# Kernel optimization log

Hardware: AMD Instinct MI355X
Metric: run time of the kernel (lower is better)

The kernel has to match this reference:

```python
import jax, jax.numpy as jnp
import numpy as np

C = 512
H_HEADS = 8  # self-attn heads (num_heads) and cross-attn heads (n_heads), both 8


def _self_attn(x, Wq, Wkv):
    # x: [B,N,C]; shared (ModuleParallel) linear weights, qkv_bias=False
    B, N, _ = x.shape
    h, d = H_HEADS, C // H_HEADS
    q = (x @ Wq.T).reshape(B, N, h, d).transpose(0, 2, 1, 3)          # [B,h,N,d]
    kv = (x @ Wkv.T).reshape(B, N, 2, h, d).transpose(2, 0, 3, 1, 4)  # [2,B,h,N,d]
    k, v = kv[0], kv[1]
    attn = jax.nn.softmax(jnp.einsum('bhnd,bhmd->bhnm', q, k) * (d ** -0.5), axis=-1)
    y = jnp.einsum('bhnm,bhmd->bhnd', attn, v).transpose(0, 2, 1, 3).reshape(B, N, C)
    return y


def _judger(y_self, y_other, Wj1, bj1, Wj2, bj2):
    # Mlp_2(2C->C->C) with exact GELU, then softmax over channel dim
    hdn = jax.nn.gelu(jnp.concatenate([y_self, y_other], axis=-1) @ Wj1.T + bj1, approximate=False)
    return jax.nn.softmax(hdn @ Wj2.T + bj2, axis=-1)


def _cross_attn(yq, ykv, kn_row, vn_row, Win, bin_, Wout, bout, rel):
    # Vectorized form of the per-sample loop: each token is a seq-len-1 query
    # attending over 2 keys: [noise_k + yq, yq * relation_score].
    B, N, _ = yq.shape
    h, d = H_HEADS, C // H_HEADS
    qw, kw, vw = Win[:C], Win[C:2 * C], Win[2 * C:]
    bq, bk, bv = bin_[:C], bin_[C:2 * C], bin_[2 * C:]
    k_in = jnp.stack([kn_row + yq, yq * rel], axis=-2)   # [B,N,2,C]
    v_in = jnp.stack([vn_row + yq, ykv], axis=-2)        # [B,N,2,C]
    qp = (yq @ qw.T + bq).reshape(B, N, h, d)
    kp = (k_in @ kw.T + bk).reshape(B, N, 2, h, d)
    vp = (v_in @ vw.T + bv).reshape(B, N, 2, h, d)
    scores = jnp.einsum('bnhd,bnkhd->bnhk', qp, kp) * (d ** -0.5)
    w = jax.nn.softmax(scores, axis=-1)
    o = jnp.einsum('bnhk,bnkhd->bnhd', w, vp).reshape(B, N, C)
    return o @ Wout.T + bout


def setup_inputs() -> dict:
    key = jax.random.key(0)
    ks = jax.random.split(key, 16)
    B, N = 8, 1024
    s = 0.02
    inp = {
        'x0': jax.random.normal(ks[0], (B, N, C), jnp.float32),
        'x1': jax.random.normal(ks[1], (B, N, C), jnp.float32),
        'H': 32, 'W': 32,
        'Wq': jax.random.normal(ks[2], (C, C), jnp.float32) * s,
        'Wkv': jax.random.normal(ks[3], (2 * C, C), jnp.float32) * s,
        'Wj1': jax.random.normal(ks[4], (C, 2 * C), jnp.float32) * s,
        'bj1': jnp.zeros((C,), jnp.float32),
        'Wj2': jax.random.normal(ks[5], (C, C), jnp.float32) * s,
        'bj2': jnp.zeros((C,), jnp.float32),
        'kn': jax.random.normal(ks[6], (2, C), jnp.float32),
        'vn': jax.random.normal(ks[7], (2, C), jnp.float32),
        'Wc0_in': jax.random.normal(ks[8], (3 * C, C), jnp.float32) * s,
        'bc0_in': jnp.zeros((3 * C,), jnp.float32),
        'Wc0_out': jax.random.normal(ks[9], (C, C), jnp.float32) * s,
        'bc0_out': jnp.zeros((C,), jnp.float32),
        'Wc1_in': jax.random.normal(ks[10], (3 * C, C), jnp.float32) * s,
        'bc1_in': jnp.zeros((3 * C,), jnp.float32),
        'Wc1_out': jax.random.normal(ks[11], (C, C), jnp.float32) * s,
        'bc1_out': jnp.zeros((C,), jnp.float32),
        'Wp': jax.random.normal(ks[12], (C, C), jnp.float32) * s,
        'bp': jnp.zeros((C,), jnp.float32),
    }
    return inp


def reference(x0, x1, H, W, Wq, Wkv, Wj1, bj1, Wj2, bj2, kn, vn,
              Wc0_in, bc0_in, Wc0_out, bc0_out, Wc1_in, bc1_in, Wc1_out, bc1_out,
              Wp, bp):
    # Dual self-attention (shared q/kv projections across modalities, sr_ratio=1)
    y0 = _self_attn(x0, Wq, Wkv)
    y1 = _self_attn(x1, Wq, Wkv)
    # Noise-augmented relation-gated cross-attention (vectorized over batch)
    rel0 = _judger(y0, y1, Wj1, bj1, Wj2, bj2)
    rel1 = _judger(y1, y0, Wj1, bj1, Wj2, bj2)
    new0 = y0 + _cross_attn(y0, y1, kn[0], vn[0], Wc0_in, bc0_in, Wc0_out, bc0_out, rel0)
    new1 = y1 + _cross_attn(y1, y0, kn[1], vn[1], Wc1_in, bc1_in, Wc1_out, bc1_out, rel1)
    out0 = new0 @ Wp.T + bp
    out1 = new1 @ Wp.T + bp
    return jnp.stack([out0, out1])  # [2,B,N,C]
```

## Files before the change

### kernel.cpp

```cpp
#include <hip/hip_runtime.h>

typedef unsigned short u16;
typedef u16 u16x8 __attribute__((ext_vector_type(8)));
typedef __bf16 bf16x8 __attribute__((ext_vector_type(8)));
typedef __bf16 bf16x2 __attribute__((ext_vector_type(2)));
typedef float f32x4 __attribute__((ext_vector_type(4)));

__device__ __forceinline__ float b2f(u16 h) {
  union { unsigned u; float f; } x; x.u = ((unsigned)h) << 16; return x.f;
}
__device__ __forceinline__ u16 f2b(float f) {
  union { float f; unsigned u; } x; x.f = f;
  unsigned r = x.u + 0x7FFFu + ((x.u >> 16) & 1u);
  return (u16)(r >> 16);
}
__device__ __forceinline__ f32x4 mfma16(bf16x8 a, bf16x8 b, f32x4 c) {
  return __builtin_amdgcn_mfma_f32_16x16x32_bf16(a, b, c, 0, 0, 0);
}
__device__ __forceinline__ void gload16(const void* g, void* l) {
  __builtin_amdgcn_global_load_lds(
      (const __attribute__((address_space(1))) void*)g,
      (__attribute__((address_space(3))) void*)l, 16, 0, 0);
}
#define WAITV8 asm volatile("s_waitcnt vmcnt(8)" ::: "memory")
#define WAITV4 asm volatile("s_waitcnt vmcnt(4)" ::: "memory")
#define WAITV0 asm volatile("s_waitcnt vmcnt(0)" ::: "memory")
#define WAITL0 asm volatile("s_waitcnt lgkmcnt(0)" ::: "memory")
#define BARRIER asm volatile("s_barrier" ::: "memory")

__global__ __launch_bounds__(256) void xcvt_k(const float* __restrict__ x0,
                                              const float* __restrict__ x1,
                                              u16* __restrict__ out) {
  int b = blockIdx.x;
  const float* src = (b < 4096) ? x0 : x1;
  u16* dst = out + (b < 4096 ? 0 : 4194304);
  int i = (b & 4095) * 1024 + threadIdx.x * 4;
  float4 v = *(const float4*)&src[i];
  dst[i + 0] = f2b(v.x); dst[i + 1] = f2b(v.y);
  dst[i + 2] = f2b(v.z); dst[i + 3] = f2b(v.w);
}

__global__ __launch_bounds__(256) void wcvt_k(
    const float* __restrict__ wq, const float* __restrict__ wkv,
    const float* __restrict__ wj1, const float* __restrict__ wj2,
    const float* __restrict__ wci0, const float* __restrict__ wci1,
    const float* __restrict__ wp, u16* __restrict__ wsb) {
  int b = blockIdx.x; const float* src; size_t doff; int lb;
  if      (b < 256)  { src = wq;   doff = 0;       lb = b; }
  else if (b < 768)  { src = wkv;  doff = 262144;  lb = b - 256; }
  else if (b < 1280) { src = wj1;  doff = 786432;  lb = b - 768; }
  else if (b < 1536) { src = wj2;  doff = 1310720; lb = b - 1280; }
  else if (b < 2304) { src = wci0; doff = 1572864; lb = b - 1536; }
  else if (b < 3072) { src = wci1; doff = 2359296; lb = b - 2304; }
  else               { src = wp;   doff = 3145728; lb = b - 3072; }
  int i = lb * 1024 + threadIdx.x * 4;
  float4 v = *(const float4*)&src[i];
  u16* dst = wsb + doff + i;
  u16 c0 = f2b(v.x), c1 = f2b(v.y), c2 = f2b(v.z), c3 = f2b(v.w);
  dst[0] = c0; dst[1] = c1; dst[2] = c2; dst[3] = c3;
  if (b >= 3072) {
    int row = i >> 9, col = i & 511;
    u16* f0 = wsb + 3932160 + (size_t)row * 1024 + col;
    u16* f1 = wsb + 4456448 + (size_t)row * 1024 + col;
    f0[0] = c0; f0[1] = c1; f0[2] = c2; f0[3] = c3;
    f1[0] = c0; f1[1] = c1; f1[2] = c2; f1[3] = c3;
  }
}

__global__ __launch_bounds__(256) void tcvt_k(const float* __restrict__ w0,
                                              const float* __restrict__ w1,
                                              u16* __restrict__ o0,
                                              u16* __restrict__ o1) {
  __shared__ u16 t[64][65];
  const int b = blockIdx.x;
  const float* src = (b & 64) ? w1 : w0;
  u16* dst = (b & 64) ? o1 : o0;
  const int r0 = ((b >> 3) & 7) * 64, c0 = (b & 7) * 64;
  const int tid = threadIdx.x;
#pragma unroll
  for (int i = 0; i < 16; i++) {
    int idx = tid + i * 256;
    int r = idx >> 6, c = idx & 63;
    t[r][c] = f2b(src[(size_t)(r0 + r) * 512 + c0 + c]);
  }
  __syncthreads();
#pragma unroll
  for (int i = 0; i < 16; i++) {
    int idx = tid + i * 256;
    int c = idx >> 6, r = idx & 63;
    dst[(size_t)(c0 + c) * 512 + r0 + r] = t[r][c];
  }
}

__global__ __launch_bounds__(256) void cvec_k(
    const float* __restrict__ kn, const float* __restrict__ vn,
    const float* __restrict__ bp, const float* __restrict__ bco0,
    const float* __restrict__ bco1, const u16* __restrict__ wci0,
    const u16* __restrict__ wci1, const u16* __restrict__ wp,
    float* __restrict__ out) {
  int idx = blockIdx.x * 256 + threadIdx.x;
  int which = idx >> 9, col = idx & 511;
  const float* src; const u16* w; float acc;
  if (which < 4) {
    int s = which & 1, isv = which >> 1;
    src = (isv ? vn : kn) + s * 512;
    w = (s ? wci1 : wci0) + (isv ? 524288 : 262144) + (size_t)col * 512;
    acc = 0.f;
  } else {
    int s = which & 1;
    src = s ? bco1 : bco0;
    w = wp + (size_t)col * 512;
    acc = bp[col];
  }
  for (int k = 0; k < 512; k += 8) {
    u16x8 w8 = *(const u16x8*)&w[k];
#pragma unroll
    for (int j = 0; j < 8; j++) acc += src[k + j] * b2f(w8[j]);
  }
  out[idx] = acc;
}

template<int EPI, int AMODE>
__global__ __launch_bounds__(256, 3) void gemm6_k(
    const u16* __restrict__ A, int astr, int K1, int K,
    const u16* __restrict__ W0, const u16* __restrict__ W1,
    const float* __restrict__ b0, const float* __restrict__ b1,
    void* __restrict__ outp, int ostr, int ncol) {
  __shared__ u16 SM[32768];
  const int tid = threadIdx.x, lane = tid & 63, wv = tid >> 6;
  const int wr = wv >> 1, wc = wv & 1;
  const int lr = lane & 15, lg = lane >> 4;
  const int L = blockIdx.x;
  const int nrow = gridDim.x / ncol;
  int row_b, col_b;
  if ((nrow & 7) == 0) {
    int xcd = L & 7, s = L >> 3;
    row_b = xcd * (nrow >> 3) + s / ncol;
    col_b = s % ncol;
  } else { row_b = L % nrow; col_b = L / nrow; }
  const int row0 = row_b * 128, col0 = col_b * 128;
  const int strm = (row0 >= 8192) ? 1 : 0;
  const u16* W = strm ? W1 : W0;
  const float* bias = strm ? b1 : b0;
  const int shift = (AMODE == 4 && col0 >= 1536) ? 512 : 0;
  const int cxor  = (AMODE == 4 && col0 >= 1536) ? 8192 : 0;
  const int bcl = (lane & 7) * 16;

  f32x4 acc[4][4];
#pragma unroll
  for (int m = 0; m < 4; m++)
#pragma unroll
    for (int n = 0; n < 4; n++) acc[m][n] = f32x4{0.f, 0.f, 0.f, 0.f};

  const int nk = K >> 6;

  auto stage = [&](int k0, int buf) {
    const int Ab = buf * 16384, Wb = buf * 16384 + 8192;
#pragma unroll
    for (int ch = 0; ch < 4; ch++) {
      int r = ch * 32 + (tid >> 3);
      int bcs = bcl ^ ((r & 7) << 4);
      const char* asrc;
      if constexpr (AMODE == 3) {
        if (k0 < K1)
          asrc = (const char*)(A + (size_t)(row0 + r) * astr) + k0 * 2 + bcs;
        else
          asrc = (const char*)(A + (size_t)((row0 + r) ^ 8192) * astr) +
                 (k0 - K1) * 2 + bcs;
      } else {
        asrc = (const char*)(A + (size_t)((row0 + r) ^ cxor) * astr) +
               k0 * 2 + bcs;
      }
      gload16(asrc, &SM[Ab + (ch * 32 + wv * 8) * 64]);
      const char* wsrc =
          (const char*)(W + (size_t)(col0 - shift + r) * K) + k0 * 2 + bcs;
      gload16(wsrc, &SM[Wb + (ch * 32 + wv * 8) * 64]);
    }
  };

  stage(0, 0);
  for (int t = 0; t < nk; t++) {
    const int buf = t & 1;
    if (t + 1 < nk) {
      stage((t + 1) * 64, buf ^ 1);
      WAITV8;
    } else {
      WAITV0;
    }
    BARRIER;
    const int Ab = buf * 16384, Wb = buf * 16384 + 8192;
#pragma unroll
    for (int kk = 0; kk < 2; kk++) {
      const int c = kk * 32 + lg * 8;
      bf16x8 af[4], wf[4];
#pragma unroll
      for (int m = 0; m < 4; m++) {
        int r = wr * 64 + m * 16 + lr;
        af[m] = *(const bf16x8*)&SM[Ab + r * 64 + (c ^ ((r & 7) << 3))];
      }
#pragma unroll
      for (int n = 0; n < 4; n++) {
        int r = wc * 64 + n * 16 + lr;
        wf[n] = *(const bf16x8*)&SM[Wb + r * 64 + (c ^ ((r & 7) << 3))];
      }
#pragma unroll
      for (int m = 0; m < 4; m++)
#pragma unroll
        for (int n = 0; n < 4; n++)
          acc[m][n] = mfma16(af[m], wf[n], acc[m][n]);
    }
    WAITL0;
    BARRIER;
  }

#pragma unroll
  for (int m = 0; m < 4; m++)
#pragma unroll
    for (int n = 0; n < 4; n++)
#pragma unroll
      for (int r = 0; r < 4; r++) {
        int grow = row0 + wr * 64 + m * 16 + lg * 4 + r;
        int gcol = col0 + wc * 64 + n * 16 + lr;
        float v = acc[m][n][r];
        if (bias) v += bias[gcol - shift];
        if (EPI == 1) v = 0.5f * v * (1.0f + erff(v * 0.70710678118f));
        if (EPI == 3) ((float*)outp)[(size_t)grow * ostr + gcol] = v;
        else          ((u16*)outp)[(size_t)grow * ostr + gcol] = f2b(v);
      }
}

__global__ __launch_bounds__(256) void vtrans_k(const u16* __restrict__ QKV,
                                                u16* __restrict__ VT) {
  __shared__ u16 t[64][66];
  const int tid = threadIdx.x;
  const int bh = blockIdx.y;
  const int sb = bh >> 3, h = bh & 7;
  const int n0 = blockIdx.x * 64;
#pragma unroll
  for (int i = 0; i < 16; i++) {
    int idx = tid + i * 256;
    int r = idx >> 6, c = idx & 63;
    t[r][c] = QKV[((size_t)sb * 1024 + n0 + r) * 1536 + 1024 + h * 64 + c];
  }
  __syncthreads();
#pragma unroll
  for (int i = 0; i < 16; i++) {
    int idx = tid + i * 256;
    int r = idx >> 6, p = idx & 63;
    int tok = ((p >> 5) << 5) + ((p & 31) >> 1) + ((p & 1) << 4);
    VT[((size_t)bh * 64 + r) * 1024 + n0 + p] = t[tok][r];
  }
}

__global__ __launch_bounds__(256) void attn_k(const u16* __restrict__ QKV,
                                              const u16* __restrict__ VT,
                                              u16* __restrict__ OC) {
  __shared__ u16 SM[24576];
  const int STR = 1536;
  const int tid = threadIdx.x, lane = tid & 63, wv = tid >> 6;
  const int lr = lane & 15, lg = lane >> 4;
  const int L = blockIdx.x;
  const int by = L & 127;
  const int q0 = (L >> 7) * 128;
  const int sb = by >> 3, h = by & 7;
  const size_t rowbase = (size_t)sb * 1024;
  const int bcl = (lane & 7) * 16;
  const float SC = 0.18033688f;

  bf16x8 qa[2][2];
#pragma unroll
  for (int m = 0; m < 2; m++)
#pragma unroll
    for (int kk = 0; kk < 2; kk++) {
      int r = q0 + wv * 32 + m * 16 + lr;
      int c = h * 64 + kk * 32 + lg * 8;
      qa[m][kk] = *(const bf16x8*)&QKV[(rowbase + r) * STR + c];
    }

  f32x4 o[2][4];
#pragma unroll
  for (int m = 0; m < 2; m++)
#pragma unroll
    for (int n = 0; n < 4; n++) o[m][n] = f32x4{0.f, 0.f, 0.f, 0.f};
  float ls[2][4] = {{0.f, 0.f, 0.f, 0.f}, {0.f, 0.f, 0.f, 0.f}};

  auto stagekv = [&](int c0, int buf) {
#pragma unroll
    for (int ch = 0; ch < 2; ch++) {
      int r = ch * 32 + (tid >> 3);
      int bcs = bcl ^ ((r & 7) << 4);
      const char* ks =
          (const char*)(QKV + (rowbase + c0 + r) * STR + 512 + h * 64) + bcs;
      gload16(ks, &SM[buf * 8192 + (ch * 32 + wv * 8) * 64]);
      const char* vs =
          (const char*)(VT + ((size_t)by * 64 + r) * 1024 + c0) + bcs;
      gload16(vs, &SM[buf * 8192 + 4096 + (ch * 32 + wv * 8) * 64]);
    }
  };

  stagekv(0, 0);
  for (int t = 0; t < 16; t++) {
    const int buf = t & 1;
    if (t < 15) {
      stagekv((t + 1) * 64, buf ^ 1);
      WAITV4;
    } else {
      WAITV0;
    }
    BARRIER;
    const int Kb = buf * 8192, Vb = buf * 8192 + 4096;

    f32x4 s[2][4];
#pragma unroll
    for (int m = 0; m < 2; m++)
#pragma unroll
      for (int n = 0; n < 4; n++) s[m][n] = f32x4{0.f, 0.f, 0.f, 0.f};
#pragma unroll
    for (int kk = 0; kk < 2; kk++) {
      const int c = kk * 32 + lg * 8;
      bf16x8 kf[4];
#pragma unroll
      for (int n = 0; n < 4; n++) {
        int r = n * 16 + lr;
        kf[n] = *(const bf16x8*)&SM[Kb + r * 64 + (c ^ ((r & 7) << 3))];
      }
#pragma unroll
      for (int m = 0; m < 2; m++)
#pragma unroll
        for (int n = 0; n < 4; n++) s[m][n] = mfma16(qa[m][kk], kf[n], s[m][n]);
    }
#pragma unroll
    for (int m = 0; m < 2; m++)
#pragma unroll
      for (int r = 0; r < 4; r++) {
        int prow = wv * 32 + m * 16 + lg * 4 + r;
        float p00 = __builtin_amdgcn_exp2f(s[m][0][r] * SC);
        float p01 = __builtin_amdgcn_exp2f(s[m][1][r] * SC);
        float p10 = __builtin_amdgcn_exp2f(s[m][2][r] * SC);
        float p11 = __builtin_amdgcn_exp2f(s[m][3][r] * SC);
        ls[m][r] += (p00 + p01) + (p10 + p11);
        bf16x2 w0; w0[0] = (__bf16)p00; w0[1] = (__bf16)p01;
        bf16x2 w1; w1[0] = (__bf16)p10; w1[1] = (__bf16)p11;
        int ib = 16384 + prow * 64, xr = (prow & 7) << 3;
        *(bf16x2*)&SM[ib + ((lr * 2) ^ xr)] = w0;
        *(bf16x2*)&SM[ib + ((32 + lr * 2) ^ xr)] = w1;
      }
#pragma unroll
    for (int kc = 0; kc < 2; kc++) {
      const int cc = kc * 32 + lg * 8;
      bf16x8 pa[2], vf[4];
#pragma unroll
      for (int m = 0; m < 2; m++) {
        int r = wv * 32 + m * 16 + lr;
        pa[m] = *(const bf16x8*)&SM[16384 + r * 64 + (cc ^ ((r & 7) << 3))];
      }
#pragma unroll
      for (int n = 0; n < 4; n++) {
        int r = n * 16 + lr;
        vf[n] = *(const bf16x8*)&SM[Vb + r * 64 + (cc ^ ((r & 7) << 3))];
      }
#pragma unroll
      for (int m = 0; m < 2; m++)
#pragma unroll
        for (int n = 0; n < 4; n++) o[m][n] = mfma16(pa[m], vf[n], o[m][n]);
    }
    WAITL0;
    BARRIER;
  }

#pragma unroll
  for (int m = 0; m < 2; m++)
#pragma unroll
    for (int r = 0; r < 4; r++) {
      float v = ls[m][r];
      v += __shfl_xor(v, 1); v += __shfl_xor(v, 2);
      v += __shfl_xor(v, 4); v += __shfl_xor(v, 8);
      ls[m][r] = v;
    }
#pragma unroll
  for (int m = 0; m < 2; m++)
#pragma unroll
    for (int n = 0; n < 4; n++)
#pragma unroll
      for (int r = 0; r < 4; r++) {
        int grow = q0 + wv * 32 + m * 16 + lg * 4 + r;
        int gcol = h * 64 + n * 16 + lr;
        OC[(rowbase + grow) * 1024 + gcol] = f2b(o[m][n][r] / ls[m][r]);
      }
}

__global__ __launch_bounds__(256) void relmul_k(const u16* __restrict__ RL,
                                                const u16* __restrict__ OC,
                                                u16* __restrict__ YKR) {
  const int row = blockIdx.x * 4 + (threadIdx.x >> 6);
  const int lane = threadIdx.x & 63;
  u16x8 lv = *(const u16x8*)&RL[(size_t)row * 512 + lane * 8];
  float e[8]; float s = 0.f;
#pragma unroll
  for (int j = 0; j < 8; j++) { e[j] = __expf(b2f(lv[j])); s += e[j]; }
  for (int x = 1; x < 64; x <<= 1) s += __shfl_xor(s, x);
  float inv = 1.0f / s;
  u16x8 y8 = *(const u16x8*)&OC[(size_t)row * 1024 + lane * 8];
  u16x8 o8;
#pragma unroll
  for (int j = 0; j < 8; j++) o8[j] = f2b(b2f(y8[j]) * (e[j] * inv));
  *(u16x8*)&YKR[(size_t)row * 512 + lane * 8] = o8;
}

__global__ __launch_bounds__(256) void twokey3_k(const u16* __restrict__ CP,
                                                 const u16* __restrict__ KP1,
                                                 const float* __restrict__ cvec,
                                                 u16* __restrict__ OC) {
  const int t = blockIdx.x * 4 + (threadIdx.x >> 6);
  const int lane = threadIdx.x & 63;
  const int s = t >> 13;
  const size_t rb = (size_t)t * 2048 + lane * 8;
  u16x8 q8 = *(const u16x8*)&CP[rb];
  u16x8 a8 = *(const u16x8*)&CP[rb + 512];
  u16x8 v0 = *(const u16x8*)&CP[rb + 1024];
  u16x8 v1 = *(const u16x8*)&CP[rb + 1536];
  u16x8 b8 = *(const u16x8*)&KP1[(size_t)t * 512 + lane * 8];
  const float* ck = cvec + s * 512 + lane * 8;
  const float* cv = cvec + 1024 + s * 512 + lane * 8;

  float s0 = 0.f, s1 = 0.f;
#pragma unroll
  for (int j = 0; j < 8; j++) {
    float qf = b2f(q8[j]);
    s0 += qf * (b2f(a8[j]) + ck[j]);
    s1 += qf * b2f(b8[j]);
  }
  s0 += __shfl_xor(s0, 1); s1 += __shfl_xor(s1, 1);
  s0 += __shfl_xor(s0, 2); s1 += __shfl_xor(s1, 2);
  s0 += __shfl_xor(s0, 4); s1 += __shfl_xor(s1, 4);

  float e0 = __expf(s0 * 0.125f), e1 = __expf(s1 * 0.125f);
  float rr = 1.0f / (e0 + e1);
  float w0 = e0 * rr, w1 = e1 * rr;
  u16x8 o8;
#pragma unroll
  for (int j = 0; j < 8; j++)
    o8[j] = f2b(w0 * (b2f(v0[j]) + cv[j]) + w1 * b2f(v1[j]));
  *(u16x8*)&OC[(size_t)t * 1024 + 512 + lane * 8] = o8;
}

extern "C" void kernel_launch(void* const* d_in, const int* in_sizes, int n_in,
                              void* d_out, int out_size, void* d_ws, size_t ws_size,
                              hipStream_t stream) {
  (void)in_sizes; (void)n_in; (void)out_size; (void)ws_size;
  const float* x0  = (const float*)d_in[0];
  const float* x1  = (const float*)d_in[1];
  const float* Wq  = (const float*)d_in[4];
  const float* Wkv = (const float*)d_in[5];
  const float* Wj1 = (const float*)d_in[6];
  const float* bj1 = (const float*)d_in[7];
  const float* Wj2 = (const float*)d_in[8];
  const float* bj2 = (const float*)d_in[9];
  const float* kn  = (const float*)d_in[10];
  const float* vn  = (const float*)d_in[11];
  const float* Wci[2]  = {(const float*)d_in[12], (const float*)d_in[16]};
  const float* bci[2]  = {(const float*)d_in[13], (const float*)d_in[17]};
  const float* Wco[2]  = {(const float*)d_in[14], (const float*)d_in[18]};
  const float* bco[2]  = {(const float*)d_in[15], (const float*)d_in[19]};
  const float* Wp  = (const float*)d_in[20];
  const float* bp  = (const float*)d_in[21];

  u16* wsb = (u16*)d_ws;
  u16* wqb   = wsb;
  u16* wj1b  = wsb + 786432;
  u16* wj2b  = wsb + 1310720;
  u16* wcib[2] = {wsb + 1572864, wsb + 2359296};
  u16* wpb   = wsb + 3145728;
  u16* wcoT[2] = {wsb + 3407872, wsb + 3670016};
  u16* wfin[2] = {wsb + 3932160, wsb + 4456448};
  float* cvecb = (float*)(wsb + 4980736);
  const size_t SLOT = 8388608;
  u16* base = wsb + 5242880;
  u16* S0 = base;
  u16* OC = base + 1 * SLOT;
  u16* S3 = base + 3 * SLOT;
  u16* S4 = base + 4 * SLOT;
  u16* S6 = base + 6 * SLOT;
  u16* QKV = S3;
  u16* REL = S3;
  u16* CP  = S3;
  u16* YKR = S4;

  dim3 blk(256);
  xcvt_k<<<dim3(8192), blk, 0, stream>>>(x0, x1, S0);
  wcvt_k<<<dim3(3328), blk, 0, stream>>>(Wq, Wkv, Wj1, Wj2, Wci[0], Wci[1],
                                         Wp, wsb);
  tcvt_k<<<dim3(128), blk, 0, stream>>>(Wco[0], Wco[1], wcoT[0], wcoT[1]);
  cvec_k<<<dim3(12), blk, 0, stream>>>(kn, vn, bp, bco[0], bco[1],
                                       wcib[0], wcib[1], wpb, cvecb);
  for (int s = 0; s < 2; s++)
    gemm6_k<0, 0><<<dim3(16), blk, 0, stream>>>(
        wpb, 512, 512, 512, wcoT[s], wcoT[s], nullptr, nullptr,
        wfin[s] + 512, 1024, 4);

  gemm6_k<0, 0><<<dim3(1536), blk, 0, stream>>>(
      S0, 512, 512, 512, wqb, wqb, nullptr, nullptr, QKV, 1536, 12);
  vtrans_k<<<dim3(16, 128), blk, 0, stream>>>(QKV, S6);
  attn_k<<<dim3(1024), blk, 0, stream>>>(QKV, S6, OC);

  gemm6_k<1, 3><<<dim3(512), blk, 0, stream>>>(
      OC, 1024, 512, 1024, wj1b, wj1b, bj1, bj1, S0, 512, 4);
  gemm6_k<0, 0><<<dim3(512), blk, 0, stream>>>(
      S0, 512, 512, 512, wj2b, wj2b, bj2, bj2, REL, 512, 4);
  relmul_k<<<dim3(4096), blk, 0, stream>>>(REL, OC, YKR);
  gemm6_k<0, 0><<<dim3(512), blk, 0, stream>>>(
      YKR, 512, 512, 512, wcib[0] + 262144, wcib[1] + 262144,
      bci[0] + 512, bci[1] + 512, S0, 512, 4);
  gemm6_k<0, 4><<<dim3(2048), blk, 0, stream>>>(
      OC, 1024, 512, 512, wcib[0], wcib[1], bci[0], bci[1], CP, 2048, 16);

  twokey3_k<<<dim3(4096), blk, 0, stream>>>(CP, S0, cvecb, OC);

  gemm6_k<3, 0><<<dim3(512), blk, 0, stream>>>(
      OC, 1024, 1024, 1024, wfin[0], wfin[1], cvecb + 2048, cvecb + 2560,
      d_out, 512, 4);
}
```

Baseline: 347.6 us.

## Enlarge GEMM tiles to 256-row blocks with 512-thread workgroups

Replaces the 128x128 GEMM kernel with a templated version that uses 256-row tiles and 128- or 256-column tiles. The workgroup grows to 8 waves, and each wave now computes 4 or 8 row fragments by 4 column fragments. Larger tiles raise data reuse per LDS load and cut global reloads of A and W. A fragments are now loaded one at a time inside the m loop. In exchange, the grid has fewer blocks, LDS use per block is higher, and register pressure rises for the MREP=8 variant, which can lower occupancy or leave CUs idle on the small GEMMs.

Result: faster. 339.4 us (-2.4%).

```diff
diff --git a/kernel.cpp b/kernel.cpp
--- a/kernel.cpp
+++ b/kernel.cpp
@@ -23,6 +23,7 @@
       (__attribute__((address_space(3))) void*)l, 16, 0, 0);
 }
 #define WAITV8 asm volatile("s_waitcnt vmcnt(8)" ::: "memory")
+#define WAITV6 asm volatile("s_waitcnt vmcnt(6)" ::: "memory")
 #define WAITV4 asm volatile("s_waitcnt vmcnt(4)" ::: "memory")
 #define WAITV0 asm volatile("s_waitcnt vmcnt(0)" ::: "memory")
 #define WAITL0 asm volatile("s_waitcnt lgkmcnt(0)" ::: "memory")
@@ -120,15 +121,19 @@
   out[idx] = acc;
 }
 
-template<int EPI, int AMODE>
-__global__ __launch_bounds__(256, 3) void gemm6_k(
+template<int EPI, int AMODE, int MREP>
+__global__ __launch_bounds__(512, 2) void gemm7_k(
     const u16* __restrict__ A, int astr, int K1, int K,
     const u16* __restrict__ W0, const u16* __restrict__ W1,
     const float* __restrict__ b0, const float* __restrict__ b1,
     void* __restrict__ outp, int ostr, int ncol) {
-  __shared__ u16 SM[32768];
+  constexpr int NW = (MREP == 8) ? 4 : 2;
+  constexpr int BN = NW * 64;
+  constexpr int BCH = BN / 64;
+  constexpr int NLD = 4 + BCH;
+  __shared__ u16 SM[32768 + BN * 128];
   const int tid = threadIdx.x, lane = tid & 63, wv = tid >> 6;
-  const int wr = wv >> 1, wc = wv & 1;
+  const int wr = wv / NW, wc = wv % NW;
   const int lr = lane & 15, lg = lane >> 4;
   const int L = blockIdx.x;
   const int nrow = gridDim.x / ncol;
@@ -138,27 +143,28 @@
     row_b = xcd * (nrow >> 3) + s / ncol;
     col_b = s % ncol;
   } else { row_b = L % nrow; col_b = L / nrow; }
-  const int row0 = row_b * 128, col0 = col_b * 128;
+  const int row0 = row_b * 256, col0 = col_b * BN;
   const int strm = (row0 >= 8192) ? 1 : 0;
   const u16* W = strm ? W1 : W0;
   const float* bias = strm ? b1 : b0;
   const int shift = (AMODE == 4 && col0 >= 1536) ? 512 : 0;
   const int cxor  = (AMODE == 4 && col0 >= 1536) ? 8192 : 0;
   const int bcl = (lane & 7) * 16;
-
-  f32x4 acc[4][4];
-#pragma unroll
-  for (int m = 0; m < 4; m++)
+  const int rT = tid >> 3;
+
+  f32x4 acc[MREP][4];
+#pragma unroll
+  for (int m = 0; m < MREP; m++)
 #pragma unroll
     for (int n = 0; n < 4; n++) acc[m][n] = f32x4{0.f, 0.f, 0.f, 0.f};
 
   const int nk = K >> 6;
 
   auto stage = [&](int k0, int buf) {
-    const int Ab = buf * 16384, Wb = buf * 16384 + 8192;
+    const int Ab = buf * 16384, Bb = 32768 + buf * (BN * 64);
 #pragma unroll
     for (int ch = 0; ch < 4; ch++) {
-      int r = ch * 32 + (tid >> 3);
+      int r = ch * 64 + rT;
       int bcs = bcl ^ ((r & 7) << 4);
       const char* asrc;
       if constexpr (AMODE == 3) {
@@ -171,10 +177,15 @@
         asrc = (const char*)(A + (size_t)((row0 + r) ^ cxor) * astr) +
                k0 * 2 + bcs;
       }
-      gload16(asrc, &SM[Ab + (ch * 32 + wv * 8) * 64]);
+      gload16(asrc, &SM[Ab + (ch * 64 + wv * 8) * 64]);
+    }
+#pragma unroll
+    for (int ch = 0; ch < BCH; ch++) {
+      int r = ch * 64 + rT;
+      int bcs = bcl ^ ((r & 7) << 4);
       const char* wsrc =
           (const char*)(W + (size_t)(col0 - shift + r) * K) + k0 * 2 + bcs;
-      gload16(wsrc, &SM[Wb + (ch * 32 + wv * 8) * 64]);
+      gload16(wsrc, &SM[Bb + (ch * 64 + wv * 8) * 64]);
     }
   };
 
@@ -183,43 +194,41 @@
     const int buf = t & 1;
     if (t + 1 < nk) {
       stage((t + 1) * 64, buf ^ 1);
-      WAITV8;
+      if constexpr (MREP == 8) { WAITV8; } else { WAITV6; }
     } else {
       WAITV0;
     }
     BARRIER;
-    const int Ab = buf * 16384, Wb = buf * 16384 + 8192;
+    const int Ab = buf * 16384, Bb = 32768 + buf * (BN * 64);
 #pragma unroll
     for (int kk = 0; kk < 2; kk++) {
       const int c = kk * 32 + lg * 8;
-      bf16x8 af[4], wf[4];
-#pragma unroll
-      for (int m = 0; m < 4; m++) {
-        int r = wr * 64 + m * 16 + lr;
-        af[m] = *(const bf16x8*)&SM[Ab + r * 64 + (c ^ ((r & 7) << 3))];
-      }
+      bf16x8 wf[4];
 #pragma unroll
       for (int n = 0; n < 4; n++) {
         int r = wc * 64 + n * 16 + lr;
-        wf[n] = *(const bf16x8*)&SM[Wb + r * 64 + (c ^ ((r & 7) << 3))];
-      }
-#pragma unroll
-      for (int m = 0; m < 4; m++)
+        wf[n] = *(const bf16x8*)&SM[Bb + r * 64 + (c ^ ((r & 7) << 3))];
+      }
+#pragma unroll
+      for (int m = 0; m < MREP; m++) {
+        int r = wr * (MREP * 16) + m * 16 + lr;
+        bf16x8 af = *(const bf16x8*)&SM[Ab + r * 64 + (c ^ ((r & 7) << 3))];
 #pragma unroll
         for (int n = 0; n < 4; n++)
-          acc[m][n] = mfma16(af[m], wf[n], acc[m][n]);
+          acc[m][n] = mfma16(af, wf[n], acc[m][n]);
+      }
     }
     WAITL0;
     BARRIER;
   }
 
 #pragma unroll
-  for (int m = 0; m < 4; m++)
+  for (int m = 0; m < MREP; m++)
 #pragma unroll
     for (int n = 0; n < 4; n++)
 #pragma unroll
       for (int r = 0; r < 4; r++) {
-        int grow = row0 + wr * 64 + m * 16 + lg * 4 + r;
+        int grow = row0 + wr * (MREP * 16) + m * 16 + lg * 4 + r;
         int gcol = col0 + wc * 64 + n * 16 + lr;
         float v = acc[m][n][r];
         if (bias) v += bias[gcol - shift];
@@ -486,7 +495,7 @@
   u16* CP  = S3;
   u16* YKR = S4;
 
-  dim3 blk(256);
+  dim3 blk(256), gblk(512);
   xcvt_k<<<dim3(8192), blk, 0, stream>>>(x0, x1, S0);
   wcvt_k<<<dim3(3328), blk, 0, stream>>>(Wq, Wkv, Wj1, Wj2, Wci[0], Wci[1],
                                          Wp, wsb);
@@ -494,29 +503,29 @@
   cvec_k<<<dim3(12), blk, 0, stream>>>(kn, vn, bp, bco[0], bco[1],
                                        wcib[0], wcib[1], wpb, cvecb);
   for (int s = 0; s < 2; s++)
-    gemm6_k<0, 0><<<dim3(16), blk, 0, stream>>>(
+    gemm7_k<0, 0, 4><<<dim3(8), gblk, 0, stream>>>(
         wpb, 512, 512, 512, wcoT[s], wcoT[s], nullptr, nullptr,
         wfin[s] + 512, 1024, 4);
 
-  gemm6_k<0, 0><<<dim3(1536), blk, 0, stream>>>(
-      S0, 512, 512, 512, wqb, wqb, nullptr, nullptr, QKV, 1536, 12);
+  gemm7_k<0, 0, 8><<<dim3(384), gblk, 0, stream>>>(
+      S0, 512, 512, 512, wqb, wqb, nullptr, nullptr, QKV, 1536, 6);
   vtrans_k<<<dim3(16, 128), blk, 0, stream>>>(QKV, S6);
   attn_k<<<dim3(1024), blk, 0, stream>>>(QKV, S6, OC);
 
-  gemm6_k<1, 3><<<dim3(512), blk, 0, stream>>>(
+  gemm7_k<1, 3, 4><<<dim3(256), gblk, 0, stream>>>(
       OC, 1024, 512, 1024, wj1b, wj1b, bj1, bj1, S0, 512, 4);
-  gemm6_k<0, 0><<<dim3(512), blk, 0, stream>>>(
+  gemm7_k<0, 0, 4><<<dim3(256), gblk, 0, stream>>>(
       S0, 512, 512, 512, wj2b, wj2b, bj2, bj2, REL, 512, 4);
   relmul_k<<<dim3(4096), blk, 0, stream>>>(REL, OC, YKR);
-  gemm6_k<0, 0><<<dim3(512), blk, 0, stream>>>(
+  gemm7_k<0, 0, 4><<<dim3(256), gblk, 0, stream>>>(
       YKR, 512, 512, 512, wcib[0] + 262144, wcib[1] + 262144,
       bci[0] + 512, bci[1] + 512, S0, 512, 4);
-  gemm6_k<0, 4><<<dim3(2048), blk, 0, stream>>>(
-      OC, 1024, 512, 512, wcib[0], wcib[1], bci[0], bci[1], CP, 2048, 16);
+  gemm7_k<0, 4, 8><<<dim3(512), gblk, 0, stream>>>(
+      OC, 1024, 512, 512, wcib[0], wcib[1], bci[0], bci[1], CP, 2048, 8);
 
   twokey3_k<<<dim3(4096), blk, 0, stream>>>(CP, S0, cvecb, OC);
 
-  gemm6_k<3, 0><<<dim3(512), blk, 0, stream>>>(
+  gemm7_k<3, 0, 4><<<dim3(256), gblk, 0, stream>>>(
       OC, 1024, 1024, 1024, wfin[0], wfin[1], cvecb + 2048, cvecb + 2560,
       d_out, 512, 4);
 }
```
